# Performance work log

Hardware: AMD Instinct MI355X
Metric: run time of the kernel (lower is better)

## Reference

```python
import jax, jax.numpy as jnp
import numpy as np

B, N, C, H = 2, 2048, 768, 12
D = C // H
HID = 4 * C  # 3072
EPS = 1e-5
PAD = 128  # last PAD key positions are padded


def _layer_norm(x, w, b):
    m = jnp.mean(x, axis=-1, keepdims=True)
    v = jnp.var(x, axis=-1, keepdims=True)
    return (x - m) * jax.lax.rsqrt(v + EPS) * w + b


def setup_inputs() -> dict:
    key = jax.random.key(0)
    ks = jax.random.split(key, 12)
    s = 0.02
    inp = {
        'x': jax.random.normal(ks[0], (B, N, C), jnp.float32),
        # keys at positions >= N-PAD are padded (mask must have some True to be exercised)
        'padding_mask': jnp.broadcast_to(jnp.arange(N) >= N - PAD, (B, N)),
        'alibi_bias': jax.random.normal(ks[1], (B, H, N, N), jnp.float32) * 0.1,
        'qkv_w': jax.random.normal(ks[2], (3 * C, C), jnp.float32) * s,
        'qkv_b': jnp.zeros((3 * C,), jnp.float32),
        'proj_w': jax.random.normal(ks[3], (C, C), jnp.float32) * s,
        'proj_b': jnp.zeros((C,), jnp.float32),
        'norm1_w': jnp.ones((C,), jnp.float32),
        'norm1_b': jnp.zeros((C,), jnp.float32),
        'norm2_w': jnp.ones((C,), jnp.float32),
        'norm2_b': jnp.zeros((C,), jnp.float32),
        'fc1_w': jax.random.normal(ks[4], (HID, C), jnp.float32) * s,
        'fc1_b': jnp.zeros((HID,), jnp.float32),
        'fc2_w': jax.random.normal(ks[5], (C, HID), jnp.float32) * s,
        'fc2_b': jnp.zeros((C,), jnp.float32),
    }
    return inp


def _attention(x, padding_mask, alibi_bias, qkv_w, qkv_b, proj_w, proj_b):
    scale = D ** (-0.5)
    qkv = (x @ qkv_w.T + qkv_b).reshape(B, N, 3, H, D).transpose(2, 0, 3, 1, 4)
    q, k, v = qkv[0] * scale, qkv[1], qkv[2]  # [B,H,N,D]
    attn = jnp.einsum('bhnd,bhmd->bhnm', q, k)
    attn = attn + alibi_bias  # alibi covers all heads here
    attn = jnp.where(padding_mask[:, None, None, :], -jnp.inf, attn)
    attn = jax.nn.softmax(attn.astype(jnp.float32), axis=-1).astype(x.dtype)
    out = jnp.einsum('bhnm,bhmd->bhnd', attn, v)
    out = out.transpose(0, 2, 1, 3).reshape(B, N, C)
    return out @ proj_w.T + proj_b


def _mlp(x, fc1_w, fc1_b, fc2_w, fc2_b):
    h = jax.nn.gelu(x @ fc1_w.T + fc1_b, approximate=False)
    return h @ fc2_w.T + fc2_b


def reference(x, padding_mask, alibi_bias, qkv_w, qkv_b, proj_w, proj_b,
              norm1_w, norm1_b, norm2_w, norm2_b, fc1_w, fc1_b, fc2_w, fc2_b):
    # layer_norm_first=True, eval mode (dropouts/drop_path = identity)
    h = x + _attention(_layer_norm(x, norm1_w, norm1_b), padding_mask, alibi_bias,
                       qkv_w, qkv_b, proj_w, proj_b)
    # Faithful to source quirk: `r = x = self.mlp(self.norm2(x))` drops the residual,
    # so output = mlp_out + mlp_out and t = mlp_out.
    t = _mlp(_layer_norm(h, norm2_w, norm2_b), fc1_w, fc1_b, fc2_w, fc2_b)
    return (t + t, t)
```

## Files before the change

kernel.cpp:

```cpp
#include <hip/hip_runtime.h>
#include <cstdint>
#include <cstddef>

#define B_   2
#define N_   2048
#define C_   768
#define H_   12
#define D_   64
#define HID_ 3072
#define BH_  24
#define MM   4096

typedef __attribute__((ext_vector_type(8))) short s16x8;
typedef __attribute__((ext_vector_type(4))) short s16x4;
typedef __attribute__((ext_vector_type(4))) float f32x4;

__device__ __forceinline__ short f2bf(float f) {
  uint32_t u = __float_as_uint(f);
  u += 0x7fffu + ((u >> 16) & 1u);
  return (short)(u >> 16);
}

__device__ __forceinline__ void gl_lds16(const void* g, void* l) {
  __builtin_amdgcn_global_load_lds((const __attribute__((address_space(1))) void*)g,
                                   (__attribute__((address_space(3))) void*)l,
                                   16, 0, 0);
}

__global__ __launch_bounds__(256) void k_cvt(const float* __restrict__ in,
                                             short* __restrict__ out, int n) {
  int i = (blockIdx.x * 256 + threadIdx.x) * 4;
  if (i >= n) return;
  float4 v = *(const float4*)(in + i);
  s16x4 o;
  o[0] = f2bf(v.x); o[1] = f2bf(v.y); o[2] = f2bf(v.z); o[3] = f2bf(v.w);
  *(s16x4*)(out + i) = o;
}

__global__ __launch_bounds__(256) void k_ln(const float* __restrict__ x,
                                            const float* __restrict__ w,
                                            const float* __restrict__ b,
                                            short* __restrict__ out) {
  const int row = blockIdx.x, t = threadIdx.x;
  const float* xr = x + (size_t)row * C_;
  float a0 = xr[t], a1 = xr[t + 256], a2 = xr[t + 512];
  float s = a0 + a1 + a2;
  float q = a0 * a0 + a1 * a1 + a2 * a2;
  #pragma unroll
  for (int off = 32; off >= 1; off >>= 1) {
    s += __shfl_xor(s, off);
    q += __shfl_xor(q, off);
  }
  __shared__ float ps[4], pq[4];
  if ((t & 63) == 0) { ps[t >> 6] = s; pq[t >> 6] = q; }
  __syncthreads();
  s = ps[0] + ps[1] + ps[2] + ps[3];
  q = pq[0] + pq[1] + pq[2] + pq[3];
  const float mean = s * (1.0f / C_);
  const float var  = q * (1.0f / C_) - mean * mean;
  const float rs   = rsqrtf(var + 1e-5f);
  short* orow = out + (size_t)row * C_;
  orow[t]       = f2bf((a0 - mean) * rs * w[t]       + b[t]);
  orow[t + 256] = f2bf((a1 - mean) * rs * w[t + 256] + b[t + 256]);
  orow[t + 512] = f2bf((a2 - mean) * rs * w[t + 512] + b[t + 512]);
}

__device__ __forceinline__ void gemm_core(const short* __restrict__ A,
                                          const short* __restrict__ Bw,
                                          int K, short* As, short* Bs,
                                          f32x4 acc[4][4]) {
  const int tid = threadIdx.x, lane = tid & 63, wid = tid >> 6;
  const int wm = wid & 1, wn = wid >> 1;
  const int l15 = lane & 15, quad = lane >> 4;
  const size_t bm = (size_t)blockIdx.x * 128, bn = (size_t)blockIdx.y * 128;
  #pragma unroll
  for (int mi = 0; mi < 4; ++mi)
    #pragma unroll
    for (int ni = 0; ni < 4; ++ni)
      acc[mi][ni] = (f32x4){0.f, 0.f, 0.f, 0.f};
  const int rrow = lane >> 2;
  const int rcol = (lane & 3) * 8;
  for (int k0 = 0; k0 < K; k0 += 32) {
    #pragma unroll
    for (int i = 0; i < 2; ++i) {
      const int rg = wid * 2 + i;
      gl_lds16(A  + (bm + rg * 16 + rrow) * (size_t)K + k0 + rcol, As + rg * 512);
      gl_lds16(Bw + (bn + rg * 16 + rrow) * (size_t)K + k0 + rcol, Bs + rg * 512);
    }
    __syncthreads();
    s16x8 af[4], bf[4];
    #pragma unroll
    for (int mi = 0; mi < 4; ++mi)
      af[mi] = *(const s16x8*)(As + (wm * 64 + mi * 16 + l15) * 32 + quad * 8);
    #pragma unroll
    for (int ni = 0; ni < 4; ++ni)
      bf[ni] = *(const s16x8*)(Bs + (wn * 64 + ni * 16 + l15) * 32 + quad * 8);
    #pragma unroll
    for (int mi = 0; mi < 4; ++mi)
      #pragma unroll
      for (int ni = 0; ni < 4; ++ni)
        acc[mi][ni] = __builtin_amdgcn_mfma_f32_16x16x32_bf16(af[mi], bf[ni],
                                                              acc[mi][ni], 0, 0, 0);
    __syncthreads();
  }
}

__global__ __launch_bounds__(256) void k_gemm_qkv(const short* __restrict__ A,
    const short* __restrict__ W, const float* __restrict__ bias,
    short* __restrict__ qb, short* __restrict__ kb, short* __restrict__ vb) {
  __shared__ short As[4096], Bs[4096];
  f32x4 acc[4][4];
  gemm_core(A, W, C_, As, Bs, acc);
  const int lane = threadIdx.x & 63, wid = threadIdx.x >> 6;
  const int wm = wid & 1, wn = wid >> 1, quad = lane >> 4, l15 = lane & 15;
  const int m0 = blockIdx.x * 128 + wm * 64;
  const int n0 = blockIdx.y * 128 + wn * 64;
  #pragma unroll
  for (int ni = 0; ni < 4; ++ni) {
    const int n = n0 + ni * 16 + l15;
    const int s = n / C_, rem = n % C_;
    const int h = rem >> 6, d = rem & 63;
    short* dst = (s == 0) ? qb : (s == 1) ? kb : vb;
    const float scale = (s == 0) ? 0.125f : 1.0f;
    const float bv = bias[n];
    #pragma unroll
    for (int mi = 0; mi < 4; ++mi)
      #pragma unroll
      for (int r = 0; r < 4; ++r) {
        const int m = m0 + mi * 16 + quad * 4 + r;
        const int bb = m >> 11, pos = m & 2047;
        dst[(((size_t)bb * H_ + h) * N_ + pos) * D_ + d] =
            f2bf((acc[mi][ni][r] + bv) * scale);
      }
  }
}

__global__ __launch_bounds__(256) void k_trans_v(const short* __restrict__ v,
                                                 short* __restrict__ vt) {
  __shared__ short t[64][68];
  const int bh = blockIdx.y;
  const int p0 = blockIdx.x * 64;
  #pragma unroll
  for (int i = 0; i < 16; ++i) {
    const int idx = threadIdx.x + i * 256;
    const int r = idx >> 6, c = idx & 63;
    t[r][c] = v[((size_t)bh * N_ + p0 + r) * D_ + c];
  }
  __syncthreads();
  #pragma unroll
  for (int i = 0; i < 16; ++i) {
    const int idx = threadIdx.x + i * 256;
    const int r = idx >> 6, c = idx & 63;
    vt[((size_t)bh * D_ + r) * N_ + p0 + c] = t[c][r];
  }
}

__global__ __launch_bounds__(256) void k_attn(const short* __restrict__ qb,
    const short* __restrict__ kb, const short* __restrict__ vtb,
    const float* __restrict__ alibi, const int* __restrict__ mask,
    short* __restrict__ aout) {
  __shared__ short Ks[64 * 72], Vs[64 * 72];
  const int tid = threadIdx.x, lane = tid & 63, wid = tid >> 6;
  const int quad = lane >> 4, l15 = lane & 15;
  const int bh = blockIdx.y, bb = bh / H_, hh = bh % H_;
  const int qg = blockIdx.x * 64 + wid * 16 + l15;

  const short* qrow = qb + ((size_t)bh * N_ + qg) * D_;
  const s16x8 qf0 = *(const s16x8*)(qrow + quad * 8);
  const s16x8 qf1 = *(const s16x8*)(qrow + 32 + quad * 8);

  f32x4 oacc[4];
  #pragma unroll
  for (int i = 0; i < 4; ++i) oacc[i] = (f32x4){0.f, 0.f, 0.f, 0.f};
  float mrun = -1e30f, lrun = 0.f;

  const float* arow = alibi + ((size_t)bh * N_ + qg) * N_;
  const int* mrow = mask + bb * N_;

  for (int jt = 0; jt < N_; jt += 64) {
    #pragma unroll
    for (int c = 0; c < 2; ++c) {
      const int idx = tid + c * 256;
      const int row = idx >> 3, col = (idx & 7) * 8;
      *(int4*)(&Ks[row * 72 + col]) =
          *(const int4*)(kb + ((size_t)bh * N_ + jt + row) * D_ + col);
      *(int4*)(&Vs[row * 72 + col]) =
          *(const int4*)(vtb + ((size_t)bh * D_ + row) * N_ + jt + col);
    }
    __syncthreads();

    int4 mk[4];
    int anyvalid = 0;
    #pragma unroll
    for (int ji = 0; ji < 4; ++ji) {
      mk[ji] = *(const int4*)(mrow + jt + ji * 16 + quad * 4);
      if (!(mk[ji].x && mk[ji].y && mk[ji].z && mk[ji].w)) anyvalid = 1;
    }
    if (!__any(anyvalid)) { __syncthreads(); continue; }

    f32x4 s[4];
    #pragma unroll
    for (int ji = 0; ji < 4; ++ji) {
      const s16x8 ka = *(const s16x8*)(&Ks[(ji * 16 + l15) * 72 + quad * 8]);
      const s16x8 kc = *(const s16x8*)(&Ks[(ji * 16 + l15) * 72 + 32 + quad * 8]);
      f32x4 z = (f32x4){0.f, 0.f, 0.f, 0.f};
      z = __builtin_amdgcn_mfma_f32_16x16x32_bf16(ka, qf0, z, 0, 0, 0);
      s[ji] = __builtin_amdgcn_mfma_f32_16x16x32_bf16(kc, qf1, z, 0, 0, 0);
    }

    float p[4][4];
    float mt = -1e30f;
    #pragma unroll
    for (int ji = 0; ji < 4; ++ji) {
      const float4 al = *(const float4*)(arow + jt + ji * 16 + quad * 4);
      float v0 = s[ji][0] + al.x; if (mk[ji].x) v0 = -1e30f;
      float v1 = s[ji][1] + al.y; if (mk[ji].y) v1 = -1e30f;
      float v2 = s[ji][2] + al.z; if (mk[ji].z) v2 = -1e30f;
      float v3 = s[ji][3] + al.w; if (mk[ji].w) v3 = -1e30f;
      p[ji][0] = v0; p[ji][1] = v1; p[ji][2] = v2; p[ji][3] = v3;
      mt = fmaxf(mt, fmaxf(fmaxf(v0, v1), fmaxf(v2, v3)));
    }
    mt = fmaxf(mt, __shfl_xor(mt, 16));
    mt = fmaxf(mt, __shfl_xor(mt, 32));
    const float mnew = fmaxf(mrun, mt);
    const float scl = __expf(mrun - mnew);
    float psum = 0.f;
    s16x4 pf[4];
    #pragma unroll
    for (int ji = 0; ji < 4; ++ji)
      #pragma unroll
      for (int r = 0; r < 4; ++r) {
        const float e = __expf(p[ji][r] - mnew);
        psum += e;
        pf[ji][r] = f2bf(e);
      }
    psum += __shfl_xor(psum, 16);
    psum += __shfl_xor(psum, 32);
    lrun = lrun * scl + psum;
    mrun = mnew;
    #pragma unroll
    for (int i = 0; i < 4; ++i) oacc[i] *= scl;

    #pragma unroll
    for (int ji = 0; ji < 4; ++ji)
      #pragma unroll
      for (int ni = 0; ni < 4; ++ni) {
        const s16x4 vf = *(const s16x4*)(&Vs[(ni * 16 + l15) * 72 + ji * 16 + quad * 4]);
        oacc[ni] = __builtin_amdgcn_mfma_f32_16x16x16bf16_1k(vf, pf[ji],
                                                             oacc[ni], 0, 0, 0);
      }
    __syncthreads();
  }

  const float inv = 1.0f / lrun;
  short* orow = aout + ((size_t)bb * N_ + qg) * C_ + hh * D_;
  #pragma unroll
  for (int ni = 0; ni < 4; ++ni)
    #pragma unroll
    for (int r = 0; r < 4; ++r)
      orow[ni * 16 + quad * 4 + r] = f2bf(oacc[ni][r] * inv);
}

__global__ __launch_bounds__(256) void k_gemm_proj(const short* __restrict__ A,
    const short* __restrict__ W, const float* __restrict__ bias,
    const float* __restrict__ xres, float* __restrict__ hout) {
  __shared__ short As[4096], Bs[4096];
  f32x4 acc[4][4];
  gemm_core(A, W, C_, As, Bs, acc);
  const int lane = threadIdx.x & 63, wid = threadIdx.x >> 6;
  const int wm = wid & 1, wn = wid >> 1, quad = lane >> 4, l15 = lane & 15;
  const int m0 = blockIdx.x * 128 + wm * 64;
  const int n0 = blockIdx.y * 128 + wn * 64;
  #pragma unroll
  for (int ni = 0; ni < 4; ++ni) {
    const int n = n0 + ni * 16 + l15;
    const float bv = bias[n];
    #pragma unroll
    for (int mi = 0; mi < 4; ++mi)
      #pragma unroll
      for (int r = 0; r < 4; ++r) {
        const int m = m0 + mi * 16 + quad * 4 + r;
        hout[(size_t)m * C_ + n] = acc[mi][ni][r] + bv + xres[(size_t)m * C_ + n];
      }
  }
}

__global__ __launch_bounds__(256) void k_gemm_fc1(const short* __restrict__ A,
    const short* __restrict__ W, const float* __restrict__ bias,
    short* __restrict__ hid) {
  __shared__ short As[4096], Bs[4096];
  f32x4 acc[4][4];
  gemm_core(A, W, C_, As, Bs, acc);
  const int lane = threadIdx.x & 63, wid = threadIdx.x >> 6;
  const int wm = wid & 1, wn = wid >> 1, quad = lane >> 4, l15 = lane & 15;
  const int m0 = blockIdx.x * 128 + wm * 64;
  const int n0 = blockIdx.y * 128 + wn * 64;
  #pragma unroll
  for (int ni = 0; ni < 4; ++ni) {
    const int n = n0 + ni * 16 + l15;
    const float bv = bias[n];
    #pragma unroll
    for (int mi = 0; mi < 4; ++mi)
      #pragma unroll
      for (int r = 0; r < 4; ++r) {
        const int m = m0 + mi * 16 + quad * 4 + r;
        const float v = acc[mi][ni][r] + bv;
        const float g = 0.5f * v * (1.0f + erff(v * 0.7071067811865475f));
        hid[(size_t)m * HID_ + n] = f2bf(g);
      }
  }
}

__global__ __launch_bounds__(256) void k_gemm_fc2(const short* __restrict__ A,
    const short* __restrict__ W, const float* __restrict__ bias,
    float* __restrict__ out) {
  __shared__ short As[4096], Bs[4096];
  f32x4 acc[4][4];
  gemm_core(A, W, HID_, As, Bs, acc);
  const int lane = threadIdx.x & 63, wid = threadIdx.x >> 6;
  const int wm = wid & 1, wn = wid >> 1, quad = lane >> 4, l15 = lane & 15;
  const int m0 = blockIdx.x * 128 + wm * 64;
  const int n0 = blockIdx.y * 128 + wn * 64;
  #pragma unroll
  for (int ni = 0; ni < 4; ++ni) {
    const int n = n0 + ni * 16 + l15;
    const float bv = bias[n];
    #pragma unroll
    for (int mi = 0; mi < 4; ++mi)
      #pragma unroll
      for (int r = 0; r < 4; ++r) {
        const int m = m0 + mi * 16 + quad * 4 + r;
        const float t = acc[mi][ni][r] + bv;
        out[(size_t)m * C_ + n] = t + t;
        out[(size_t)MM * C_ + (size_t)m * C_ + n] = t;
      }
  }
}

extern "C" void kernel_launch(void* const* d_in, const int* in_sizes, int n_in,
                              void* d_out, int out_size, void* d_ws, size_t ws_size,
                              hipStream_t stream) {
  (void)in_sizes; (void)n_in; (void)out_size; (void)ws_size;
  const float* x      = (const float*)d_in[0];
  const int*   mask   = (const int*)  d_in[1];
  const float* alibi  = (const float*)d_in[2];
  const float* qkv_w  = (const float*)d_in[3];
  const float* qkv_b  = (const float*)d_in[4];
  const float* proj_w = (const float*)d_in[5];
  const float* proj_b = (const float*)d_in[6];
  const float* n1w    = (const float*)d_in[7];
  const float* n1b    = (const float*)d_in[8];
  const float* n2w    = (const float*)d_in[9];
  const float* n2b    = (const float*)d_in[10];
  const float* fc1_w  = (const float*)d_in[11];
  const float* fc1_b  = (const float*)d_in[12];
  const float* fc2_w  = (const float*)d_in[13];
  const float* fc2_b  = (const float*)d_in[14];
  float* out = (float*)d_out;

  char* ws = (char*)d_ws;
  size_t off = 0;
  auto alloc = [&](size_t bytes) -> void* {
    void* p = ws + off;
    off += (bytes + 255) & ~(size_t)255;
    return p;
  };
  short* wq   = (short*)alloc((size_t)3 * C_ * C_ * 2);
  short* wp   = (short*)alloc((size_t)C_ * C_ * 2);
  short* wf1  = (short*)alloc((size_t)HID_ * C_ * 2);
  short* wf2  = (short*)alloc((size_t)C_ * HID_ * 2);
  short* xln  = (short*)alloc((size_t)MM * C_ * 2);
  short* qb   = (short*)alloc((size_t)BH_ * N_ * D_ * 2);
  short* kb   = (short*)alloc((size_t)BH_ * N_ * D_ * 2);
  short* vb   = (short*)alloc((size_t)BH_ * N_ * D_ * 2);
  short* vtb  = (short*)alloc((size_t)BH_ * D_ * N_ * 2);
  float* h    = (float*)alloc((size_t)MM * C_ * 4);
  short* hid  = (short*)alloc((size_t)MM * HID_ * 2);
  short* hln  = xln;
  short* aout = vb;

  k_cvt<<<3 * C_ * C_ / 1024, 256, 0, stream>>>(qkv_w, wq, 3 * C_ * C_);
  k_cvt<<<C_ * C_ / 1024, 256, 0, stream>>>(proj_w, wp, C_ * C_);
  k_cvt<<<HID_ * C_ / 1024, 256, 0, stream>>>(fc1_w, wf1, HID_ * C_);
  k_cvt<<<C_ * HID_ / 1024, 256, 0, stream>>>(fc2_w, wf2, C_ * HID_);

  k_ln<<<MM, 256, 0, stream>>>(x, n1w, n1b, xln);
  k_gemm_qkv<<<dim3(MM / 128, 3 * C_ / 128), 256, 0, stream>>>(xln, wq, qkv_b,
                                                               qb, kb, vb);
  k_trans_v<<<dim3(N_ / 64, BH_), 256, 0, stream>>>(vb, vtb);
  k_attn<<<dim3(N_ / 64, BH_), 256, 0, stream>>>(qb, kb, vtb, alibi, mask, aout);
  k_gemm_proj<<<dim3(MM / 128, C_ / 128), 256, 0, stream>>>(aout, wp, proj_b, x, h);
  k_ln<<<MM, 256, 0, stream>>>(h, n2w, n2b, hln);
  k_gemm_fc1<<<dim3(MM / 128, HID_ / 128), 256, 0, stream>>>(hln, wf1, fc1_b, hid);
  k_gemm_fc2<<<dim3(MM / 128, C_ / 128), 256, 0, stream>>>(hid, wf2, fc2_b, out);
}
```

Baseline: 787.7 us.

## Split-K proj and fc2 GEMMs, fuse weight casts, tanh GELU, early mask skip

Adds 2-way and 4-way split-K to the undersized proj and fc2 GEMM grids, with separate reduction kernels that apply bias, residual and output duplication. Merges the four weight conversion launches into one. Replaces the erf GELU with a tanh-based approximation. Moves the attention padding-mask check ahead of the K/V tile loads so fully masked tiles skip the loads and barriers. In exchange, it writes and reads extra fp32 partial buffers, and the GELU approximation deviates from the exact reference.

```diff
diff --git a/kernel.cpp b/kernel.cpp
--- a/kernel.cpp
+++ b/kernel.cpp
@@ -27,10 +27,25 @@
                                    16, 0, 0);
 }
 
-__global__ __launch_bounds__(256) void k_cvt(const float* __restrict__ in,
-                                             short* __restrict__ out, int n) {
-  int i = (blockIdx.x * 256 + threadIdx.x) * 4;
-  if (i >= n) return;
+__device__ __forceinline__ float gelu_tanh(float v) {
+  const float z  = 0.7978845608f * v * (1.0f + 0.044715f * v * v);
+  const float e  = __expf(-2.0f * fabsf(z));
+  const float th = copysignf((1.0f - e) / (1.0f + e), z);
+  return 0.5f * v * (1.0f + th);
+}
+
+__global__ __launch_bounds__(256) void k_cvt4(
+    const float* __restrict__ a, short* __restrict__ oa,
+    const float* __restrict__ b, short* __restrict__ ob,
+    const float* __restrict__ c, short* __restrict__ oc,
+    const float* __restrict__ d, short* __restrict__ od) {
+  const int blk = blockIdx.x;
+  const float* in; short* out; int base;
+  if (blk < 1728)      { in = a; out = oa; base = blk; }
+  else if (blk < 2304) { in = b; out = ob; base = blk - 1728; }
+  else if (blk < 4608) { in = c; out = oc; base = blk - 2304; }
+  else                 { in = d; out = od; base = blk - 4608; }
+  const int i = (base * 256 + threadIdx.x) * 4;
   float4 v = *(const float4*)(in + i);
   s16x4 o;
   o[0] = f2bf(v.x); o[1] = f2bf(v.y); o[2] = f2bf(v.z); o[3] = f2bf(v.w);
@@ -67,7 +82,8 @@
 
 __device__ __forceinline__ void gemm_core(const short* __restrict__ A,
                                           const short* __restrict__ Bw,
-                                          int K, short* As, short* Bs,
+                                          int ldk, int kbeg, int kend,
+                                          short* As, short* Bs,
                                           f32x4 acc[4][4]) {
   const int tid = threadIdx.x, lane = tid & 63, wid = tid >> 6;
   const int wm = wid & 1, wn = wid >> 1;
@@ -80,12 +96,12 @@
       acc[mi][ni] = (f32x4){0.f, 0.f, 0.f, 0.f};
   const int rrow = lane >> 2;
   const int rcol = (lane & 3) * 8;
-  for (int k0 = 0; k0 < K; k0 += 32) {
+  for (int k0 = kbeg; k0 < kend; k0 += 32) {
     #pragma unroll
     for (int i = 0; i < 2; ++i) {
       const int rg = wid * 2 + i;
-      gl_lds16(A  + (bm + rg * 16 + rrow) * (size_t)K + k0 + rcol, As + rg * 512);
-      gl_lds16(Bw + (bn + rg * 16 + rrow) * (size_t)K + k0 + rcol, Bs + rg * 512);
+      gl_lds16(A  + (bm + rg * 16 + rrow) * (size_t)ldk + k0 + rcol, As + rg * 512);
+      gl_lds16(Bw + (bn + rg * 16 + rrow) * (size_t)ldk + k0 + rcol, Bs + rg * 512);
     }
     __syncthreads();
     s16x8 af[4], bf[4];
@@ -110,7 +126,7 @@
     short* __restrict__ qb, short* __restrict__ kb, short* __restrict__ vb) {
   __shared__ short As[4096], Bs[4096];
   f32x4 acc[4][4];
-  gemm_core(A, W, C_, As, Bs, acc);
+  gemm_core(A, W, C_, 0, C_, As, Bs, acc);
   const int lane = threadIdx.x & 63, wid = threadIdx.x >> 6;
   const int wm = wid & 1, wn = wid >> 1, quad = lane >> 4, l15 = lane & 15;
   const int m0 = blockIdx.x * 128 + wm * 64;
@@ -178,6 +194,15 @@
   const int* mrow = mask + bb * N_;
 
   for (int jt = 0; jt < N_; jt += 64) {
+    int4 mk[4];
+    int anyvalid = 0;
+    #pragma unroll
+    for (int ji = 0; ji < 4; ++ji) {
+      mk[ji] = *(const int4*)(mrow + jt + ji * 16 + quad * 4);
+      if (!(mk[ji].x && mk[ji].y && mk[ji].z && mk[ji].w)) anyvalid = 1;
+    }
+    if (!__any(anyvalid)) continue;
+
     #pragma unroll
     for (int c = 0; c < 2; ++c) {
       const int idx = tid + c * 256;
@@ -188,15 +213,6 @@
           *(const int4*)(vtb + ((size_t)bh * D_ + row) * N_ + jt + col);
     }
     __syncthreads();
-
-    int4 mk[4];
-    int anyvalid = 0;
-    #pragma unroll
-    for (int ji = 0; ji < 4; ++ji) {
-      mk[ji] = *(const int4*)(mrow + jt + ji * 16 + quad * 4);
-      if (!(mk[ji].x && mk[ji].y && mk[ji].z && mk[ji].w)) anyvalid = 1;
-    }
-    if (!__any(anyvalid)) { __syncthreads(); continue; }
 
     f32x4 s[4];
     #pragma unroll
@@ -261,28 +277,44 @@
       orow[ni * 16 + quad * 4 + r] = f2bf(oacc[ni][r] * inv);
 }
 
-__global__ __launch_bounds__(256) void k_gemm_proj(const short* __restrict__ A,
-    const short* __restrict__ W, const float* __restrict__ bias,
-    const float* __restrict__ xres, float* __restrict__ hout) {
+__global__ __launch_bounds__(256) void k_gemm_projs(const short* __restrict__ A,
+    const short* __restrict__ W, float* __restrict__ part) {
   __shared__ short As[4096], Bs[4096];
   f32x4 acc[4][4];
-  gemm_core(A, W, C_, As, Bs, acc);
+  const int z = blockIdx.z;
+  gemm_core(A, W, C_, z * 384, z * 384 + 384, As, Bs, acc);
   const int lane = threadIdx.x & 63, wid = threadIdx.x >> 6;
   const int wm = wid & 1, wn = wid >> 1, quad = lane >> 4, l15 = lane & 15;
   const int m0 = blockIdx.x * 128 + wm * 64;
   const int n0 = blockIdx.y * 128 + wn * 64;
+  float* pz = part + (size_t)z * MM * C_;
   #pragma unroll
   for (int ni = 0; ni < 4; ++ni) {
     const int n = n0 + ni * 16 + l15;
-    const float bv = bias[n];
     #pragma unroll
     for (int mi = 0; mi < 4; ++mi)
       #pragma unroll
       for (int r = 0; r < 4; ++r) {
         const int m = m0 + mi * 16 + quad * 4 + r;
-        hout[(size_t)m * C_ + n] = acc[mi][ni][r] + bv + xres[(size_t)m * C_ + n];
-      }
-  }
+        pz[(size_t)m * C_ + n] = acc[mi][ni][r];
+      }
+  }
+}
+
+__global__ __launch_bounds__(256) void k_proj_red(const float* __restrict__ p,
+    const float* __restrict__ bias, const float* __restrict__ xres,
+    float* __restrict__ hout) {
+  const int i = (blockIdx.x * 256 + threadIdx.x) * 4;
+  const float4 s0 = *(const float4*)(p + i);
+  const float4 s1 = *(const float4*)(p + (size_t)MM * C_ + i);
+  const float4 bv = *(const float4*)(bias + (i % C_));
+  const float4 xr = *(const float4*)(xres + i);
+  float4 o;
+  o.x = s0.x + s1.x + bv.x + xr.x;
+  o.y = s0.y + s1.y + bv.y + xr.y;
+  o.z = s0.z + s1.z + bv.z + xr.z;
+  o.w = s0.w + s1.w + bv.w + xr.w;
+  *(float4*)(hout + i) = o;
 }
 
 __global__ __launch_bounds__(256) void k_gemm_fc1(const short* __restrict__ A,
@@ -290,7 +322,7 @@
     short* __restrict__ hid) {
   __shared__ short As[4096], Bs[4096];
   f32x4 acc[4][4];
-  gemm_core(A, W, C_, As, Bs, acc);
+  gemm_core(A, W, C_, 0, C_, As, Bs, acc);
   const int lane = threadIdx.x & 63, wid = threadIdx.x >> 6;
   const int wm = wid & 1, wn = wid >> 1, quad = lane >> 4, l15 = lane & 15;
   const int m0 = blockIdx.x * 128 + wm * 64;
@@ -304,37 +336,50 @@
       #pragma unroll
       for (int r = 0; r < 4; ++r) {
         const int m = m0 + mi * 16 + quad * 4 + r;
-        const float v = acc[mi][ni][r] + bv;
-        const float g = 0.5f * v * (1.0f + erff(v * 0.7071067811865475f));
-        hid[(size_t)m * HID_ + n] = f2bf(g);
-      }
-  }
-}
-
-__global__ __launch_bounds__(256) void k_gemm_fc2(const short* __restrict__ A,
-    const short* __restrict__ W, const float* __restrict__ bias,
-    float* __restrict__ out) {
+        hid[(size_t)m * HID_ + n] = f2bf(gelu_tanh(acc[mi][ni][r] + bv));
+      }
+  }
+}
+
+__global__ __launch_bounds__(256) void k_gemm_fc2s(const short* __restrict__ A,
+    const short* __restrict__ W, float* __restrict__ part) {
   __shared__ short As[4096], Bs[4096];
   f32x4 acc[4][4];
-  gemm_core(A, W, HID_, As, Bs, acc);
+  const int z = blockIdx.z;
+  gemm_core(A, W, HID_, z * 768, z * 768 + 768, As, Bs, acc);
   const int lane = threadIdx.x & 63, wid = threadIdx.x >> 6;
   const int wm = wid & 1, wn = wid >> 1, quad = lane >> 4, l15 = lane & 15;
   const int m0 = blockIdx.x * 128 + wm * 64;
   const int n0 = blockIdx.y * 128 + wn * 64;
+  float* pz = part + (size_t)z * MM * C_;
   #pragma unroll
   for (int ni = 0; ni < 4; ++ni) {
     const int n = n0 + ni * 16 + l15;
-    const float bv = bias[n];
     #pragma unroll
     for (int mi = 0; mi < 4; ++mi)
       #pragma unroll
       for (int r = 0; r < 4; ++r) {
         const int m = m0 + mi * 16 + quad * 4 + r;
-        const float t = acc[mi][ni][r] + bv;
-        out[(size_t)m * C_ + n] = t + t;
-        out[(size_t)MM * C_ + (size_t)m * C_ + n] = t;
-      }
-  }
+        pz[(size_t)m * C_ + n] = acc[mi][ni][r];
+      }
+  }
+}
+
+__global__ __launch_bounds__(256) void k_fc2_red(const float* __restrict__ p,
+    const float* __restrict__ bias, float* __restrict__ out) {
+  const int i = (blockIdx.x * 256 + threadIdx.x) * 4;
+  const float4 s0 = *(const float4*)(p + i);
+  const float4 s1 = *(const float4*)(p + (size_t)MM * C_ + i);
+  const float4 s2 = *(const float4*)(p + (size_t)2 * MM * C_ + i);
+  const float4 s3 = *(const float4*)(p + (size_t)3 * MM * C_ + i);
+  const float4 bv = *(const float4*)(bias + (i % C_));
+  float4 t, t2;
+  t.x = s0.x + s1.x + s2.x + s3.x + bv.x;  t2.x = t.x + t.x;
+  t.y = s0.y + s1.y + s2.y + s3.y + bv.y;  t2.y = t.y + t.y;
+  t.z = s0.z + s1.z + s2.z + s3.z + bv.z;  t2.z = t.z + t.z;
+  t.w = s0.w + s1.w + s2.w + s3.w + bv.w;  t2.w = t.w + t.w;
+  *(float4*)(out + i) = t2;
+  *(float4*)(out + (size_t)MM * C_ + i) = t;
 }
 
 extern "C" void kernel_launch(void* const* d_in, const int* in_sizes, int n_in,
@@ -376,21 +421,22 @@
   short* vtb  = (short*)alloc((size_t)BH_ * D_ * N_ * 2);
   float* h    = (float*)alloc((size_t)MM * C_ * 4);
   short* hid  = (short*)alloc((size_t)MM * HID_ * 2);
+  float* ppj  = (float*)alloc((size_t)2 * MM * C_ * 4);
+  float* pf2  = (float*)alloc((size_t)4 * MM * C_ * 4);
   short* hln  = xln;
   short* aout = vb;
 
-  k_cvt<<<3 * C_ * C_ / 1024, 256, 0, stream>>>(qkv_w, wq, 3 * C_ * C_);
-  k_cvt<<<C_ * C_ / 1024, 256, 0, stream>>>(proj_w, wp, C_ * C_);
-  k_cvt<<<HID_ * C_ / 1024, 256, 0, stream>>>(fc1_w, wf1, HID_ * C_);
-  k_cvt<<<C_ * HID_ / 1024, 256, 0, stream>>>(fc2_w, wf2, C_ * HID_);
+  k_cvt4<<<6912, 256, 0, stream>>>(qkv_w, wq, proj_w, wp, fc1_w, wf1, fc2_w, wf2);
 
   k_ln<<<MM, 256, 0, stream>>>(x, n1w, n1b, xln);
   k_gemm_qkv<<<dim3(MM / 128, 3 * C_ / 128), 256, 0, stream>>>(xln, wq, qkv_b,
                                                                qb, kb, vb);
   k_trans_v<<<dim3(N_ / 64, BH_), 256, 0, stream>>>(vb, vtb);
   k_attn<<<dim3(N_ / 64, BH_), 256, 0, stream>>>(qb, kb, vtb, alibi, mask, aout);
-  k_gemm_proj<<<dim3(MM / 128, C_ / 128), 256, 0, stream>>>(aout, wp, proj_b, x, h);
+  k_gemm_projs<<<dim3(MM / 128, C_ / 128, 2), 256, 0, stream>>>(aout, wp, ppj);
+  k_proj_red<<<MM * C_ / 1024, 256, 0, stream>>>(ppj, proj_b, x, h);
   k_ln<<<MM, 256, 0, stream>>>(h, n2w, n2b, hln);
   k_gemm_fc1<<<dim3(MM / 128, HID_ / 128), 256, 0, stream>>>(hln, wf1, fc1_b, hid);
-  k_gemm_fc2<<<dim3(MM / 128, C_ / 128), 256, 0, stream>>>(hid, wf2, fc2_b, out);
-}
+  k_gemm_fc2s<<<dim3(MM / 128, C_ / 128, 4), 256, 0, stream>>>(hid, wf2, pf2);
+  k_fc2_red<<<MM * C_ / 1024, 256, 0, stream>>>(pf2, fc2_b, out);
+}
```

Result: faster. 749.4 us (-4.9%).
